# Kernel tuning notes

Hardware: AMD Instinct MI355X
Metric: run time of the kernel (lower is better)

## Reference

```python
import jax, jax.numpy as jnp
import numpy as np

HIDDEN = 2048
N_HEADS = 16
HEAD_DIM = HIDDEN // N_HEADS
FF_DIM = 5632  # int(2*4*2048/3)=5461 rounded up to multiple of 256
ROPE_THETA = 500000.0
NORM_EPS = 1e-5
B, S = 2, 2048


def apply_rope(x, positions, inv_freq):
    # x: [B,S,H,D], positions: [B,S], inv_freq: [D/2]
    angles = positions.astype(inv_freq.dtype)[..., None] * inv_freq[None, None, :]
    cos = jnp.cos(angles)[:, :, None, :]
    sin = jnp.sin(angles)[:, :, None, :]
    x_pair = x.reshape(*x.shape[:-1], x.shape[-1] // 2, 2)
    x0, x1 = x_pair[..., 0], x_pair[..., 1]
    out = jnp.stack([x0 * cos - x1 * sin, x1 * cos + x0 * sin], axis=-1)
    return out.reshape(x.shape).astype(x.dtype)


def rmsnorm(x, scale, eps=NORM_EPS):
    var = jnp.mean(jnp.square(x), axis=-1, keepdims=True)
    return (x * jax.lax.rsqrt(var + eps)) * scale


def setup_inputs() -> dict:
    key = jax.random.key(0)
    ks = jax.random.split(key, 12)
    sd = 1.0 / np.sqrt(HIDDEN)
    sdf = 1.0 / np.sqrt(FF_DIM)
    x = jax.random.normal(ks[0], (B, S, HIDDEN), dtype=jnp.float32)
    positions = jnp.tile(jnp.arange(S, dtype=jnp.int32)[None, :], (B, 1))
    mask = jnp.tril(jnp.ones((S, S), dtype=jnp.bool_))[None].repeat(B, axis=0)
    return {
        "x": x,
        "positions": positions,
        "mask": mask,
        "wq": jax.random.normal(ks[1], (HIDDEN, HIDDEN), jnp.float32) * sd,
        "wk": jax.random.normal(ks[2], (HIDDEN, HIDDEN), jnp.float32) * sd,
        "wv": jax.random.normal(ks[3], (HIDDEN, HIDDEN), jnp.float32) * sd,
        "wo": jax.random.normal(ks[4], (HIDDEN, HIDDEN), jnp.float32) * sd,
        "attn_scale": jnp.ones((HIDDEN,), jnp.float32),
        "ffn_scale": jnp.ones((HIDDEN,), jnp.float32),
        "w1": jax.random.normal(ks[5], (HIDDEN, FF_DIM), jnp.float32) * sd,
        "w3": jax.random.normal(ks[6], (HIDDEN, FF_DIM), jnp.float32) * sd,
        "w2": jax.random.normal(ks[7], (FF_DIM, HIDDEN), jnp.float32) * sdf,
    }


def reference(x, positions, mask, wq, wk, wv, wo, attn_scale, ffn_scale, w1, w3, w2):
    Bx = x.shape[0]
    inv_freq = 1.0 / ROPE_THETA ** (jnp.arange(0, HEAD_DIM, 2, dtype=jnp.float32) / HEAD_DIM)
    x_norm = rmsnorm(x, attn_scale)
    q = apply_rope((x_norm @ wq).reshape(Bx, -1, N_HEADS, HEAD_DIM), positions, inv_freq)
    k = apply_rope((x_norm @ wk).reshape(Bx, -1, N_HEADS, HEAD_DIM), positions, inv_freq)
    v = (x_norm @ wv).reshape(Bx, -1, N_HEADS, HEAD_DIM)
    scale = 1.0 / jnp.sqrt(jnp.float32(HEAD_DIM)).astype(q.dtype)
    # [B,H,S,S]
    attn_weights = jnp.einsum("bqhd,bkhd->bhqk", q, k) * scale
    big_neg = jnp.finfo(q.dtype).min
    attn_weights = jnp.where(mask[:, None, :, :], attn_weights, big_neg)
    attn_weights = jax.nn.softmax(attn_weights, axis=-1)
    attn_out = jnp.einsum("bhqk,bkhd->bqhd", attn_weights, v).reshape(Bx, -1, HIDDEN)
    h = x + attn_out @ wo
    ff = rmsnorm(h, ffn_scale)
    return h + (jax.nn.silu(ff @ w1) * (ff @ w3)) @ w2
```

## Files before the change

### kernel.cpp

```cpp
#include <hip/hip_runtime.h>

#define HID 2048
#define SEQ 2048
#define NB 2
#define NHD 16
#define HD 128
#define FF 5632
#define MROWS 4096

typedef __bf16 bf16x8 __attribute__((ext_vector_type(8)));
typedef float f32x4 __attribute__((ext_vector_type(4)));
typedef unsigned short u16;
typedef unsigned int u32;
typedef unsigned long long u64;

__device__ __forceinline__ u16 f2bf(float f) {
  u32 u = __float_as_uint(f);
  u += 0x7fffu + ((u >> 16) & 1u);
  return (u16)(u >> 16);
}
__device__ __forceinline__ float bf2f(u16 h) {
  return __uint_as_float(((u32)h) << 16);
}
__device__ __forceinline__ void gld16(const void* g, void* l) {
  __builtin_amdgcn_global_load_lds((__attribute__((address_space(1))) void*)g,
                                   (__attribute__((address_space(3))) void*)l, 16, 0, 0);
}

__global__ __launch_bounds__(256) void rmsnorm_k(const float* __restrict__ x,
                                                 const float* __restrict__ sc,
                                                 u16* __restrict__ out) {
  __shared__ float red[4];
  const int row = blockIdx.x, t = threadIdx.x;
  const float4* xr = (const float4*)(x + (size_t)row * HID);
  float4 a = xr[t], b = xr[t + 256];
  float ss = a.x*a.x + a.y*a.y + a.z*a.z + a.w*a.w
           + b.x*b.x + b.y*b.y + b.z*b.z + b.w*b.w;
#pragma unroll
  for (int o = 1; o < 64; o <<= 1) ss += __shfl_xor(ss, o);
  if ((t & 63) == 0) red[t >> 6] = ss;
  __syncthreads();
  float tot = red[0] + red[1] + red[2] + red[3];
  float r = rsqrtf(tot * (1.0f / HID) + 1e-5f);
  const float4* scp = (const float4*)sc;
  float4 s0 = scp[t], s1 = scp[t + 256];
  u32 p0 = (u32)f2bf(a.x*r*s0.x) | ((u32)f2bf(a.y*r*s0.y) << 16);
  u32 p1 = (u32)f2bf(a.z*r*s0.z) | ((u32)f2bf(a.w*r*s0.w) << 16);
  u32 p2 = (u32)f2bf(b.x*r*s1.x) | ((u32)f2bf(b.y*r*s1.y) << 16);
  u32 p3 = (u32)f2bf(b.z*r*s1.z) | ((u32)f2bf(b.w*r*s1.w) << 16);
  u32* op = (u32*)(out + (size_t)row * HID);
  op[t*2] = p0; op[t*2+1] = p1;
  op[512 + t*2] = p2; op[512 + t*2 + 1] = p3;
}

__global__ __launch_bounds__(256) void transpose_cvt_k(const float* __restrict__ W,
                                                       u16* __restrict__ Wt,
                                                       int R, int C) {
  __shared__ float tile[32][33];
  const int tx = threadIdx.x & 31, ty = threadIdx.x >> 5;
  const int bc = blockIdx.x * 32, br = blockIdx.y * 32;
#pragma unroll
  for (int i = 0; i < 4; ++i)
    tile[ty + i*8][tx] = W[(size_t)(br + ty + i*8) * C + bc + tx];
  __syncthreads();
#pragma unroll
  for (int i = 0; i < 4; ++i)
    Wt[(size_t)(bc + ty + i*8) * R + br + tx] = f2bf(tile[tx][ty + i*8]);
}

__global__ __launch_bounds__(256) void rope_k(u16* __restrict__ qk, const int* __restrict__ pos) {
  const u32 i = blockIdx.x * 256 + threadIdx.x;
  const int d2 = i & 63;
  const int s = (i >> 6) & 2047;
  const int bh = i >> 17;
  const int b = bh >> 4;
  const float p = (float)pos[(size_t)b * SEQ + s];
  const float ang = p * exp2f(-(float)d2 * 0.2958057589f);
  float sv, cv;
  sincosf(ang, &sv, &cv);
  u32* ptr = (u32*)(qk + ((size_t)bh * SEQ + s) * HD) + d2;
  u32 u = *ptr;
  float x0 = bf2f((u16)(u & 0xffff)), x1 = bf2f((u16)(u >> 16));
  float o0 = x0 * cv - x1 * sv;
  float o1 = x1 * cv + x0 * sv;
  *ptr = (u32)f2bf(o0) | ((u32)f2bf(o1) << 16);
}

#define VMW(N) asm volatile("s_waitcnt vmcnt(" #N ")" ::: "memory")
#define BARR() do { __builtin_amdgcn_s_barrier(); __builtin_amdgcn_sched_barrier(0); } while (0)

#define STAGE_A(NB, H) do { \
  gld16(ap + (size_t)((H)*128) * K,      &Ab[NB][(H)*8192 + wid*512]); \
  gld16(ap + (size_t)((H)*128 + 64) * K, &Ab[NB][(H)*8192 + 4096 + wid*512]); \
} while (0)
#define STAGE_B(NB, H) do { \
  gld16(bp + (size_t)((H)*128) * K,      &Bb[NB][(H)*8192 + wid*512]); \
  gld16(bp + (size_t)((H)*128 + 64) * K, &Bb[NB][(H)*8192 + 4096 + wid*512]); \
} while (0)
#define READ_A(BF, AH) do { \
  const char* pa_ = (const char*)Ab[BF] + (AH)*16384 + arow; \
  av[0][0] = *(const bf16x8*)(pa_ + 0*4096 + ck0); av[0][1] = *(const bf16x8*)(pa_ + 0*4096 + ck1); \
  av[1][0] = *(const bf16x8*)(pa_ + 1*4096 + ck0); av[1][1] = *(const bf16x8*)(pa_ + 1*4096 + ck1); \
  av[2][0] = *(const bf16x8*)(pa_ + 2*4096 + ck0); av[2][1] = *(const bf16x8*)(pa_ + 2*4096 + ck1); \
  av[3][0] = *(const bf16x8*)(pa_ + 3*4096 + ck0); av[3][1] = *(const bf16x8*)(pa_ + 3*4096 + ck1); \
} while (0)
#define READ_B(BF, BH) do { \
  const char* pb_ = (const char*)Bb[BF] + (BH)*16384 + brow; \
  bv[(BH)*2+0][0] = *(const bf16x8*)(pb_ + 0*8192 + ck0); bv[(BH)*2+0][1] = *(const bf16x8*)(pb_ + 0*8192 + ck1); \
  bv[(BH)*2+1][0] = *(const bf16x8*)(pb_ + 1*8192 + ck0); bv[(BH)*2+1][1] = *(const bf16x8*)(pb_ + 1*8192 + ck1); \
} while (0)
#define MMAQ(AH, BH) do { \
  __builtin_amdgcn_s_setprio(1); \
  _Pragma("unroll") \
  for (int kk_ = 0; kk_ < 2; ++kk_) \
    _Pragma("unroll") \
    for (int m_ = 0; m_ < 4; ++m_) \
      _Pragma("unroll") \
      for (int n_ = 0; n_ < 2; ++n_) \
        acc[(AH)*4+m_][(BH)*2+n_] = __builtin_amdgcn_mfma_f32_16x16x32_bf16( \
            av[m_][kk_], bv[(BH)*2+n_][kk_], acc[(AH)*4+m_][(BH)*2+n_], 0, 0, 0); \
  __builtin_amdgcn_s_setprio(0); \
} while (0)

template <int EPI>
__global__ __launch_bounds__(512, 2) void gemm256_k(const u16* __restrict__ A,
                                                    const u16* __restrict__ Bt,
                                                    int N, int K,
                                                    const float* __restrict__ addsrc,
                                                    const u16* __restrict__ mulsrc,
                                                    void* __restrict__ outp) {
  __shared__ __align__(16) u16 Ab[2][16384];
  __shared__ __align__(16) u16 Bb[2][16384];
  const int tid = threadIdx.x, lane = tid & 63, wid = tid >> 6;
  const int lr = lane & 15, lg = lane >> 4;
  const int wr = wid >> 2, wc = wid & 3;

  const int gx = gridDim.x;
  int bid = blockIdx.y * gx + blockIdx.x;
  const int q8 = (gx * gridDim.y) >> 3;
  bid = (bid & 7) * q8 + (bid >> 3);
  const int mt = (bid / gx) * 256, nt = (bid % gx) * 256;

  const f32x4 fz = {0.f, 0.f, 0.f, 0.f};
  f32x4 acc[8][4];
#pragma unroll
  for (int i = 0; i < 8; ++i)
#pragma unroll
    for (int j = 0; j < 4; ++j) acc[i][j] = fz;

  const int srow = tid >> 3;
  const int scol = ((((tid & 7) * 16) ^ (((srow >> 2) & 1) << 5)) >> 1);
  const u16* ap = A  + (size_t)(mt + srow) * K + scol;
  const u16* bp = Bt + (size_t)(nt + srow) * K + scol;

  const int arow = (wr * 16 + lr) * 128;
  const int brow = (wc * 16 + lr) * 128;
  const int swl = ((lr >> 2) & 1) << 5;
  const int ck0 = (lg * 16) ^ swl;
  const int ck1 = (64 + lg * 16) ^ swl;

  bf16x8 av[4][2], bv[4][2];

  STAGE_A(0, 0); STAGE_B(0, 0); STAGE_B(0, 1); STAGE_A(0, 1);
  ap += 64; bp += 64;

  const int ntk = K >> 6;
  int buf = 0;
  for (int t = 0; t < ntk - 1; ++t) {
    const int nb = buf ^ 1;
    STAGE_A(nb, 0);  VMW(6); BARR();
    READ_A(buf, 0);  READ_B(buf, 0);  MMAQ(0, 0);
    STAGE_B(nb, 0);  VMW(6); BARR();
    READ_B(buf, 1);  MMAQ(0, 1);
    STAGE_B(nb, 1);  VMW(6); BARR();
    READ_A(buf, 1);  MMAQ(1, 1);
    STAGE_A(nb, 1);
    MMAQ(1, 0);
    ap += 64; bp += 64;
    buf = nb;
  }
  VMW(4); BARR();
  READ_A(buf, 0); READ_B(buf, 0); MMAQ(0, 0);
  VMW(2); BARR();
  READ_B(buf, 1); MMAQ(0, 1);
  VMW(0); BARR();
  READ_A(buf, 1); MMAQ(1, 1);
  MMAQ(1, 0);

#pragma unroll
  for (int mi = 0; mi < 8; ++mi) {
#pragma unroll
    for (int ni = 0; ni < 4; ++ni) {
      const int gr0 = mt + mi * 32 + wr * 16 + lg * 4;
      const int gc = nt + ni * 64 + wc * 16 + lr;
      f32x4 v = acc[mi][ni];
      if (EPI == 1) {
        const int which = gc >> 11;
        const int c2 = gc & 2047;
        const int hh = c2 >> 7, d = c2 & 127;
        if (which < 2) {
          u16* dst = (u16*)outp + (size_t)which * ((size_t)MROWS * HID);
#pragma unroll
          for (int r = 0; r < 4; ++r) {
            const int gr = gr0 + r;
            const int b = gr >> 11, s = gr & 2047;
            dst[((((size_t)(b * NHD + hh)) * SEQ + s) << 7) + d] = f2bf(v[r]);
          }
        } else {
          u16* dst = (u16*)outp + (size_t)2 * ((size_t)MROWS * HID);
          const int b = gr0 >> 11, s0 = gr0 & 2047;
          u64 pk = (u64)f2bf(v[0]) | ((u64)f2bf(v[1]) << 16)
                 | ((u64)f2bf(v[2]) << 32) | ((u64)f2bf(v[3]) << 48);
          *(u64*)(dst + ((((size_t)(b * NHD + hh)) * HD + d) << 11) + s0) = pk;
        }
      } else {
#pragma unroll
        for (int r = 0; r < 4; ++r) {
          const int gr = gr0 + r;
          const float val = v[r];
          if (EPI == 2) {
            const size_t o = (size_t)gr * N + gc;
            ((float*)outp)[o] = addsrc[o] + val;
          } else if (EPI == 3) {
            const size_t o = (size_t)gr * N + gc;
            ((u16*)outp)[o] = f2bf(val / (1.f + __expf(-val)));
          } else if (EPI == 4) {
            const size_t o = (size_t)gr * N + gc;
            ((u16*)outp)[o] = f2bf(bf2f(mulsrc[o]) * val);
          }
        }
      }
    }
  }
}

#define ATT_SW(row) (((row) & 7) << 4)

__device__ __forceinline__ void att_stage(const u16* __restrict__ Kp,
                                          const u16* __restrict__ Vp,
                                          int kt, char* kb, char* vb,
                                          int tid, int wid) {
#pragma unroll
  for (int j = 0; j < 4; ++j) {
    const int c = j * 256 + tid;
    const int row = c >> 4;
    const int scb = ((c & 15) << 4) ^ ATT_SW(row);
    gld16(Kp + (size_t)(kt + row) * HD + (scb >> 1), kb + j * 4096 + wid * 1024);
  }
#pragma unroll
  for (int j = 0; j < 4; ++j) {
    const int c = j * 256 + tid;
    const int row = c >> 3;
    const int scb = ((c & 7) << 4) ^ ATT_SW(row);
    gld16(Vp + (size_t)row * SEQ + kt + (scb >> 1), vb + j * 4096 + wid * 1024);
  }
}

__global__ __launch_bounds__(256, 2) void attn_k(const u16* __restrict__ Q,
                                                 const u16* __restrict__ Kg,
                                                 const u16* __restrict__ Vtg,
                                                 u16* __restrict__ out) {
  __shared__ __align__(16) char Kb[2][16384];
  __shared__ __align__(16) char Vb[2][16384];
  __shared__ __align__(16) u16 Pl[4][16 * 72];
  const int tid = threadIdx.x, lane = tid & 63, wid = tid >> 6;
  const int lr = lane & 15, lg = lane >> 4;
  int wg = blockIdx.x;
  wg = (wg & 7) * 64 + (wg >> 3);
  const int bh = wg >> 4, pr = wg & 15;
  const size_t bhoff = (size_t)bh * SEQ * HD;
  const u16* Qp = Q + bhoff;
  const u16* Kp = Kg + bhoff;
  const u16* Vp = Vtg + bhoff;
  const int bb = bh >> 4, hh = bh & 15;
  u16* Pw = Pl[wid];
  const int sw = ATT_SW(lr);
  const float scale = 0.08838834764831845f;
  const f32x4 fz = {0.f, 0.f, 0.f, 0.f};

  for (int side = 0; side < 2; ++side) {
    const int qt = side ? (31 - pr) : pr;
    const int qrow0 = qt * 64 + wid * 16;

    bf16x8 qf[4];
#pragma unroll
    for (int t = 0; t < 4; ++t)
      qf[t] = *(const bf16x8*)(Qp + (size_t)(qrow0 + lr) * HD + t * 32 + lg * 8);

    f32x4 o[8];
#pragma unroll
    for (int i = 0; i < 8; ++i) o[i] = fz;
    float mrun[4] = {-1e30f, -1e30f, -1e30f, -1e30f};
    float lrun[4] = {0.f, 0.f, 0.f, 0.f};

    const int kend = qt * 64 + 64;
    int cur = 0;
    att_stage(Kp, Vp, 0, Kb[0], Vb[0], tid, wid);
    __syncthreads();

    for (int kt = 0; kt < kend; kt += 64) {
      if (kt + 64 < kend)
        att_stage(Kp, Vp, kt + 64, Kb[cur ^ 1], Vb[cur ^ 1], tid, wid);
      const char* kbuf = Kb[cur];
      const char* vbuf = Vb[cur];

      f32x4 sc2[4];
#pragma unroll
      for (int nh = 0; nh < 4; ++nh) {
        f32x4 s = fz;
#pragma unroll
        for (int t = 0; t < 4; ++t) {
          bf16x8 kf = *(const bf16x8*)(kbuf + (nh * 16 + lr) * 256 + ((t * 64 + lg * 16) ^ sw));
          s = __builtin_amdgcn_mfma_f32_16x16x32_bf16(qf[t], kf, s, 0, 0, 0);
        }
        sc2[nh] = s;
      }

      float pv[4][4], alpha[4];
#pragma unroll
      for (int r = 0; r < 4; ++r) {
        const int qrow = qrow0 + lg * 4 + r;
        float s0 = sc2[0][r] * scale;
        float s1 = sc2[1][r] * scale;
        float s2 = sc2[2][r] * scale;
        float s3 = sc2[3][r] * scale;
        if (kt + lr > qrow)      s0 = -1e30f;
        if (kt + 16 + lr > qrow) s1 = -1e30f;
        if (kt + 32 + lr > qrow) s2 = -1e30f;
        if (kt + 48 + lr > qrow) s3 = -1e30f;
        float mx = fmaxf(fmaxf(s0, s1), fmaxf(s2, s3));
        mx = fmaxf(mx, __shfl_xor(mx, 1));
        mx = fmaxf(mx, __shfl_xor(mx, 2));
        mx = fmaxf(mx, __shfl_xor(mx, 4));
        mx = fmaxf(mx, __shfl_xor(mx, 8));
        const float mn = fmaxf(mrun[r], mx);
        const float p0 = __expf(s0 - mn), p1 = __expf(s1 - mn);
        const float p2 = __expf(s2 - mn), p3 = __expf(s3 - mn);
        float ts = p0 + p1 + p2 + p3;
        ts += __shfl_xor(ts, 1);
        ts += __shfl_xor(ts, 2);
        ts += __shfl_xor(ts, 4);
        ts += __shfl_xor(ts, 8);
        const float al = __expf(mrun[r] - mn);
        alpha[r] = al;
        lrun[r] = lrun[r] * al + ts;
        mrun[r] = mn;
        pv[0][r] = p0; pv[1][r] = p1; pv[2][r] = p2; pv[3][r] = p3;
      }
#pragma unroll
      for (int i = 0; i < 8; ++i) {
        o[i][0] *= alpha[0]; o[i][1] *= alpha[1];
        o[i][2] *= alpha[2]; o[i][3] *= alpha[3];
      }

#pragma unroll
      for (int nh = 0; nh < 4; ++nh)
#pragma unroll
        for (int r = 0; r < 4; ++r)
          Pw[(lg * 4 + r) * 72 + nh * 16 + lr] = f2bf(pv[nh][r]);
      asm volatile("s_waitcnt lgkmcnt(0)\n" ::: "memory");
      const bf16x8 pf0 = *(const bf16x8*)(Pw + lr * 72 + lg * 8);
      const bf16x8 pf1 = *(const bf16x8*)(Pw + lr * 72 + 32 + lg * 8);

#pragma unroll
      for (int nt2 = 0; nt2 < 8; ++nt2) {
        const char* vr = vbuf + (nt2 * 16 + lr) * 128;
        bf16x8 v0 = *(const bf16x8*)(vr + ((lg * 16) ^ sw));
        bf16x8 v1 = *(const bf16x8*)(vr + ((64 + lg * 16) ^ sw));
        o[nt2] = __builtin_amdgcn_mfma_f32_16x16x32_bf16(pf0, v0, o[nt2], 0, 0, 0);
        o[nt2] = __builtin_amdgcn_mfma_f32_16x16x32_bf16(pf1, v1, o[nt2], 0, 0, 0);
      }
      __syncthreads();
      cur ^= 1;
    }

#pragma unroll
    for (int r = 0; r < 4; ++r) {
      const int q = qrow0 + lg * 4 + r;
      const float inv = 1.f / lrun[r];
      u16* op = out + ((size_t)(bb * SEQ + q)) * HID + hh * HD + lr;
#pragma unroll
      for (int nt2 = 0; nt2 < 8; ++nt2)
        op[nt2 * 16] = f2bf(o[nt2][r] * inv);
    }
  }
}

extern "C" void kernel_launch(void* const* d_in, const int* in_sizes, int n_in,
                              void* d_out, int out_size, void* d_ws, size_t ws_size,
                              hipStream_t stream) {
  (void)in_sizes; (void)n_in; (void)out_size; (void)ws_size;
  const float* x   = (const float*)d_in[0];
  const int*   pos = (const int*)d_in[1];
  const float* wq  = (const float*)d_in[3];
  const float* wk  = (const float*)d_in[4];
  const float* wv  = (const float*)d_in[5];
  const float* wo  = (const float*)d_in[6];
  const float* asc = (const float*)d_in[7];
  const float* fsc = (const float*)d_in[8];
  const float* w1  = (const float*)d_in[9];
  const float* w3  = (const float*)d_in[10];
  const float* w2  = (const float*)d_in[11];
  float* out = (float*)d_out;

  char* ws = (char*)d_ws;
  u16* qb = (u16*)ws; ws += (size_t)MROWS * HID * 2;
  u16* kb = (u16*)ws; ws += (size_t)MROWS * HID * 2;
  u16* vb = (u16*)ws; ws += (size_t)MROWS * HID * 2;
  u16* xb = (u16*)ws; ws += (size_t)MROWS * HID * 2;
  u16* gb = (u16*)ws; ws += (size_t)MROWS * FF * 2;
  u16* wb = (u16*)ws; ws += (size_t)FF * HID * 2;
  u16* wqkvT = gb;

  dim3 b256(256), b512(512);

  rmsnorm_k<<<MROWS, b256, 0, stream>>>(x, asc, xb);

  transpose_cvt_k<<<dim3(HID/32, HID/32), b256, 0, stream>>>(wq, wqkvT, HID, HID);
  transpose_cvt_k<<<dim3(HID/32, HID/32), b256, 0, stream>>>(wk, wqkvT + (size_t)HID*HID, HID, HID);
  transpose_cvt_k<<<dim3(HID/32, HID/32), b256, 0, stream>>>(wv, wqkvT + (size_t)2*HID*HID, HID, HID);
  gemm256_k<1><<<dim3(3*HID/256, MROWS/256), b512, 0, stream>>>(xb, wqkvT, 3*HID, HID, nullptr, nullptr, qb);

  rope_k<<<(NB*NHD*SEQ*(HD/2))/256, b256, 0, stream>>>(qb, pos);
  rope_k<<<(NB*NHD*SEQ*(HD/2))/256, b256, 0, stream>>>(kb, pos);

  attn_k<<<dim3(512), b256, 0, stream>>>(qb, kb, vb, xb);

  transpose_cvt_k<<<dim3(HID/32, HID/32), b256, 0, stream>>>(wo, wb, HID, HID);
  gemm256_k<2><<<dim3(HID/256, MROWS/256), b512, 0, stream>>>(xb, wb, HID, HID, x, nullptr, out);

  rmsnorm_k<<<MROWS, b256, 0, stream>>>(out, fsc, xb);

  transpose_cvt_k<<<dim3(FF/32, HID/32), b256, 0, stream>>>(w1, wb, HID, FF);
  gemm256_k<3><<<dim3(FF/256, MROWS/256), b512, 0, stream>>>(xb, wb, FF, HID, nullptr, nullptr, gb);
  transpose_cvt_k<<<dim3(FF/32, HID/32), b256, 0, stream>>>(w3, wb, HID, FF);
  gemm256_k<4><<<dim3(FF/256, MROWS/256), b512, 0, stream>>>(xb, wb, FF, HID, nullptr, gb, gb);
  transpose_cvt_k<<<dim3(HID/32, FF/32), b256, 0, stream>>>(w2, wb, FF, HID);
  gemm256_k<2><<<dim3(HID/256, MROWS/256), b512, 0, stream>>>(gb, wb, HID, FF, out, nullptr, out);
}
```

Measured before the change: 1.016 ms.

## Replace 256x256 GEMM tile with simpler 128x128 double-buffered tile

Replaces the 256x256, 512-thread GEMM, whose loads and MFMAs were interleaved in quarters, with a 128x128, 256-thread GEMM. The new kernel uses a plain double-buffered loop: wait for all loads, barrier, issue the next stage, then two MFMA groups. The LDS swizzle changes to an XOR over 8 rows. Smaller tiles give more blocks to fill the CUs but lower arithmetic intensity, and the full vmcnt(0) wait per iteration removes the finer load/compute overlap of the old schedule.

```diff
diff --git a/kernel.cpp b/kernel.cpp
--- a/kernel.cpp
+++ b/kernel.cpp
@@ -89,110 +89,97 @@
 #define VMW(N) asm volatile("s_waitcnt vmcnt(" #N ")" ::: "memory")
 #define BARR() do { __builtin_amdgcn_s_barrier(); __builtin_amdgcn_sched_barrier(0); } while (0)
 
-#define STAGE_A(NB, H) do { \
-  gld16(ap + (size_t)((H)*128) * K,      &Ab[NB][(H)*8192 + wid*512]); \
-  gld16(ap + (size_t)((H)*128 + 64) * K, &Ab[NB][(H)*8192 + 4096 + wid*512]); \
+#define STG(NB) do { \
+  gld16(ap + (size_t)0*32*K, &Ab[NB][0*2048 + wid*512]); \
+  gld16(ap + (size_t)1*32*K, &Ab[NB][1*2048 + wid*512]); \
+  gld16(ap + (size_t)2*32*K, &Ab[NB][2*2048 + wid*512]); \
+  gld16(ap + (size_t)3*32*K, &Ab[NB][3*2048 + wid*512]); \
+  gld16(bp + (size_t)0*32*K, &Bb[NB][0*2048 + wid*512]); \
+  gld16(bp + (size_t)1*32*K, &Bb[NB][1*2048 + wid*512]); \
+  gld16(bp + (size_t)2*32*K, &Bb[NB][2*2048 + wid*512]); \
+  gld16(bp + (size_t)3*32*K, &Bb[NB][3*2048 + wid*512]); \
 } while (0)
-#define STAGE_B(NB, H) do { \
-  gld16(bp + (size_t)((H)*128) * K,      &Bb[NB][(H)*8192 + wid*512]); \
-  gld16(bp + (size_t)((H)*128 + 64) * K, &Bb[NB][(H)*8192 + 4096 + wid*512]); \
+
+#define RDA(BF, CK) do { \
+  const char* pa_ = (const char*)Ab[BF] + (wr*64 + lr)*128 + (CK); \
+  av[0] = *(const bf16x8*)(pa_);          av[1] = *(const bf16x8*)(pa_ + 2048); \
+  av[2] = *(const bf16x8*)(pa_ + 4096);   av[3] = *(const bf16x8*)(pa_ + 6144); \
 } while (0)
-#define READ_A(BF, AH) do { \
-  const char* pa_ = (const char*)Ab[BF] + (AH)*16384 + arow; \
-  av[0][0] = *(const bf16x8*)(pa_ + 0*4096 + ck0); av[0][1] = *(const bf16x8*)(pa_ + 0*4096 + ck1); \
-  av[1][0] = *(const bf16x8*)(pa_ + 1*4096 + ck0); av[1][1] = *(const bf16x8*)(pa_ + 1*4096 + ck1); \
-  av[2][0] = *(const bf16x8*)(pa_ + 2*4096 + ck0); av[2][1] = *(const bf16x8*)(pa_ + 2*4096 + ck1); \
-  av[3][0] = *(const bf16x8*)(pa_ + 3*4096 + ck0); av[3][1] = *(const bf16x8*)(pa_ + 3*4096 + ck1); \
+#define RDB(BF, CK) do { \
+  const char* pb_ = (const char*)Bb[BF] + (wc*64 + lr)*128 + (CK); \
+  bv[0] = *(const bf16x8*)(pb_);          bv[1] = *(const bf16x8*)(pb_ + 2048); \
+  bv[2] = *(const bf16x8*)(pb_ + 4096);   bv[3] = *(const bf16x8*)(pb_ + 6144); \
 } while (0)
-#define READ_B(BF, BH) do { \
-  const char* pb_ = (const char*)Bb[BF] + (BH)*16384 + brow; \
-  bv[(BH)*2+0][0] = *(const bf16x8*)(pb_ + 0*8192 + ck0); bv[(BH)*2+0][1] = *(const bf16x8*)(pb_ + 0*8192 + ck1); \
-  bv[(BH)*2+1][0] = *(const bf16x8*)(pb_ + 1*8192 + ck0); bv[(BH)*2+1][1] = *(const bf16x8*)(pb_ + 1*8192 + ck1); \
-} while (0)
-#define MMAQ(AH, BH) do { \
+#define MMA16() do { \
   __builtin_amdgcn_s_setprio(1); \
   _Pragma("unroll") \
-  for (int kk_ = 0; kk_ < 2; ++kk_) \
+  for (int m_ = 0; m_ < 4; ++m_) \
     _Pragma("unroll") \
-    for (int m_ = 0; m_ < 4; ++m_) \
-      _Pragma("unroll") \
-      for (int n_ = 0; n_ < 2; ++n_) \
-        acc[(AH)*4+m_][(BH)*2+n_] = __builtin_amdgcn_mfma_f32_16x16x32_bf16( \
-            av[m_][kk_], bv[(BH)*2+n_][kk_], acc[(AH)*4+m_][(BH)*2+n_], 0, 0, 0); \
+    for (int n_ = 0; n_ < 4; ++n_) \
+      acc[m_][n_] = __builtin_amdgcn_mfma_f32_16x16x32_bf16(av[m_], bv[n_], acc[m_][n_], 0, 0, 0); \
   __builtin_amdgcn_s_setprio(0); \
 } while (0)
 
 template <int EPI>
-__global__ __launch_bounds__(512, 2) void gemm256_k(const u16* __restrict__ A,
-                                                    const u16* __restrict__ Bt,
-                                                    int N, int K,
-                                                    const float* __restrict__ addsrc,
-                                                    const u16* __restrict__ mulsrc,
-                                                    void* __restrict__ outp) {
-  __shared__ __align__(16) u16 Ab[2][16384];
-  __shared__ __align__(16) u16 Bb[2][16384];
+__global__ __launch_bounds__(256, 2) void gemm_k(const u16* __restrict__ A,
+                                                 const u16* __restrict__ Bt,
+                                                 int N, int K,
+                                                 const float* __restrict__ addsrc,
+                                                 const u16* __restrict__ mulsrc,
+                                                 void* __restrict__ outp) {
+  __shared__ __align__(16) u16 Ab[2][128 * 64];
+  __shared__ __align__(16) u16 Bb[2][128 * 64];
   const int tid = threadIdx.x, lane = tid & 63, wid = tid >> 6;
   const int lr = lane & 15, lg = lane >> 4;
-  const int wr = wid >> 2, wc = wid & 3;
+  const int wr = wid >> 1, wc = wid & 1;
 
   const int gx = gridDim.x;
   int bid = blockIdx.y * gx + blockIdx.x;
   const int q8 = (gx * gridDim.y) >> 3;
   bid = (bid & 7) * q8 + (bid >> 3);
-  const int mt = (bid / gx) * 256, nt = (bid % gx) * 256;
+  const int mt = (bid / gx) * 128, nt = (bid % gx) * 128;
 
   const f32x4 fz = {0.f, 0.f, 0.f, 0.f};
-  f32x4 acc[8][4];
-#pragma unroll
-  for (int i = 0; i < 8; ++i)
+  f32x4 acc[4][4];
+#pragma unroll
+  for (int i = 0; i < 4; ++i)
 #pragma unroll
     for (int j = 0; j < 4; ++j) acc[i][j] = fz;
 
   const int srow = tid >> 3;
-  const int scol = ((((tid & 7) * 16) ^ (((srow >> 2) & 1) << 5)) >> 1);
+  const int scol = ((((tid & 7) << 4) ^ ((srow & 7) << 4)) >> 1);
   const u16* ap = A  + (size_t)(mt + srow) * K + scol;
   const u16* bp = Bt + (size_t)(nt + srow) * K + scol;
 
-  const int arow = (wr * 16 + lr) * 128;
-  const int brow = (wc * 16 + lr) * 128;
-  const int swl = ((lr >> 2) & 1) << 5;
+  const int swl = (lr & 7) << 4;
   const int ck0 = (lg * 16) ^ swl;
   const int ck1 = (64 + lg * 16) ^ swl;
 
-  bf16x8 av[4][2], bv[4][2];
-
-  STAGE_A(0, 0); STAGE_B(0, 0); STAGE_B(0, 1); STAGE_A(0, 1);
+  bf16x8 av[4], bv[4];
+
+  STG(0);
   ap += 64; bp += 64;
 
   const int ntk = K >> 6;
   int buf = 0;
-  for (int t = 0; t < ntk - 1; ++t) {
-    const int nb = buf ^ 1;
-    STAGE_A(nb, 0);  VMW(6); BARR();
-    READ_A(buf, 0);  READ_B(buf, 0);  MMAQ(0, 0);
-    STAGE_B(nb, 0);  VMW(6); BARR();
-    READ_B(buf, 1);  MMAQ(0, 1);
-    STAGE_B(nb, 1);  VMW(6); BARR();
-    READ_A(buf, 1);  MMAQ(1, 1);
-    STAGE_A(nb, 1);
-    MMAQ(1, 0);
-    ap += 64; bp += 64;
-    buf = nb;
+  for (int t = 0; t < ntk; ++t) {
+    VMW(0);
+    BARR();
+    if (t + 1 < ntk) {
+      STG(buf ^ 1);
+      ap += 64; bp += 64;
+    }
+    RDA(buf, ck0); RDB(buf, ck0); MMA16();
+    RDA(buf, ck1); RDB(buf, ck1); MMA16();
+    buf ^= 1;
   }
-  VMW(4); BARR();
-  READ_A(buf, 0); READ_B(buf, 0); MMAQ(0, 0);
-  VMW(2); BARR();
-  READ_B(buf, 1); MMAQ(0, 1);
-  VMW(0); BARR();
-  READ_A(buf, 1); MMAQ(1, 1);
-  MMAQ(1, 0);
-
-#pragma unroll
-  for (int mi = 0; mi < 8; ++mi) {
+
+#pragma unroll
+  for (int mi = 0; mi < 4; ++mi) {
 #pragma unroll
     for (int ni = 0; ni < 4; ++ni) {
-      const int gr0 = mt + mi * 32 + wr * 16 + lg * 4;
-      const int gc = nt + ni * 64 + wc * 16 + lr;
+      const int gr0 = mt + wr * 64 + mi * 16 + lg * 4;
+      const int gc = nt + wc * 64 + ni * 16 + lr;
       f32x4 v = acc[mi][ni];
       if (EPI == 1) {
         const int which = gc >> 11;
@@ -412,14 +399,14 @@
   u16* wb = (u16*)ws; ws += (size_t)FF * HID * 2;
   u16* wqkvT = gb;
 
-  dim3 b256(256), b512(512);
+  dim3 b256(256);
 
   rmsnorm_k<<<MROWS, b256, 0, stream>>>(x, asc, xb);
 
   transpose_cvt_k<<<dim3(HID/32, HID/32), b256, 0, stream>>>(wq, wqkvT, HID, HID);
   transpose_cvt_k<<<dim3(HID/32, HID/32), b256, 0, stream>>>(wk, wqkvT + (size_t)HID*HID, HID, HID);
   transpose_cvt_k<<<dim3(HID/32, HID/32), b256, 0, stream>>>(wv, wqkvT + (size_t)2*HID*HID, HID, HID);
-  gemm256_k<1><<<dim3(3*HID/256, MROWS/256), b512, 0, stream>>>(xb, wqkvT, 3*HID, HID, nullptr, nullptr, qb);
+  gemm_k<1><<<dim3(3*HID/128, MROWS/128), b256, 0, stream>>>(xb, wqkvT, 3*HID, HID, nullptr, nullptr, qb);
 
   rope_k<<<(NB*NHD*SEQ*(HD/2))/256, b256, 0, stream>>>(qb, pos);
   rope_k<<<(NB*NHD*SEQ*(HD/2))/256, b256, 0, stream>>>(kb, pos);
@@ -427,14 +414,14 @@
   attn_k<<<dim3(512), b256, 0, stream>>>(qb, kb, vb, xb);
 
   transpose_cvt_k<<<dim3(HID/32, HID/32), b256, 0, stream>>>(wo, wb, HID, HID);
-  gemm256_k<2><<<dim3(HID/256, MROWS/256), b512, 0, stream>>>(xb, wb, HID, HID, x, nullptr, out);
+  gemm_k<2><<<dim3(HID/128, MROWS/128), b256, 0, stream>>>(xb, wb, HID, HID, x, nullptr, out);
 
   rmsnorm_k<<<MROWS, b256, 0, stream>>>(out, fsc, xb);
 
   transpose_cvt_k<<<dim3(FF/32, HID/32), b256, 0, stream>>>(w1, wb, HID, FF);
-  gemm256_k<3><<<dim3(FF/256, MROWS/256), b512, 0, stream>>>(xb, wb, FF, HID, nullptr, nullptr, gb);
+  gemm_k<3><<<dim3(FF/128, MROWS/128), b256, 0, stream>>>(xb, wb, FF, HID, nullptr, nullptr, gb);
   transpose_cvt_k<<<dim3(FF/32, HID/32), b256, 0, stream>>>(w3, wb, HID, FF);
-  gemm256_k<4><<<dim3(FF/256, MROWS/256), b512, 0, stream>>>(xb, wb, FF, HID, nullptr, gb, gb);
+  gemm_k<4><<<dim3(FF/128, MROWS/128), b256, 0, stream>>>(xb, wb, FF, HID, nullptr, gb, gb);
   transpose_cvt_k<<<dim3(HID/32, FF/32), b256, 0, stream>>>(w2, wb, FF, HID);
-  gemm256_k<2><<<dim3(HID/256, MROWS/256), b512, 0, stream>>>(gb, wb, HID, FF, out, nullptr, out);
-}
+  gemm_k<2><<<dim3(HID/128, MROWS/128), b256, 0, stream>>>(gb, wb, HID, FF, out, nullptr, out);
+}
```

Measured after the change: 877.0 us. -13.7%, faster.
